# Kernel optimization log

Measured on AMD Instinct MI355X. Metric: run time of the kernel, lower is better.

Reference implementation:

```python
import jax, jax.numpy as jnp
import numpy as np

ROPE_BASE = 10000.0
ROPE_SCALE = 1.0
ATTN_SCALE = 0.08838834764831845  # query_pre_attn_scalar = 128**-0.5
WINDOW = 1024                     # sliding_window_size
EPS = 1e-6                        # flax RMSNorm default epsilon


def rms_norm(x, scale):
    var = jnp.mean(jnp.square(x), axis=-1, keepdims=True)
    return x * jax.lax.rsqrt(var + EPS) * scale


def apply_rope(x, positions):
    # x: [B, T, n, H]; positions: [B, T]
    H = x.shape[-1]
    frac = jnp.arange(0, H, 2, dtype=jnp.float32) / H        # [H/2]
    timescale = ROPE_BASE ** frac                             # [H/2]
    sinusoid = positions[..., None].astype(jnp.float32) / timescale  # [B,T,H/2]
    sinusoid = sinusoid / ROPE_SCALE
    sin = jnp.sin(sinusoid)[:, :, None, :]                    # [B,T,1,H/2]
    cos = jnp.cos(sinusoid)[:, :, None, :]
    x1, x2 = jnp.split(x, 2, axis=-1)
    return jnp.concatenate([x1 * cos - x2 * sin, x2 * cos + x1 * sin], axis=-1).astype(x.dtype)


def setup_inputs() -> dict:
    key = jax.random.key(0)
    ks = jax.random.split(key, 4)
    B, T, D, N, K, H = 1, 4096, 2048, 16, 8, 128
    return {
        "x": jax.random.normal(ks[0], (B, T, D), jnp.float32),
        "q_kernel": jax.random.normal(ks[1], (N, D, H), jnp.float32) * (D ** -0.5),
        "kv_kernel": jax.random.normal(ks[2], (2, K, D, H), jnp.float32) * (D ** -0.5),
        "out_kernel": jax.random.normal(ks[3], (N, H, D), jnp.float32) * ((N * H) ** -0.5),
        "q_norm_scale": jnp.ones((H,), jnp.float32),
        "k_norm_scale": jnp.ones((H,), jnp.float32),
    }


def reference(x, q_kernel, kv_kernel, out_kernel, q_norm_scale, k_norm_scale):
    B, T, D = x.shape
    N, _, H = q_kernel.shape
    K = kv_kernel.shape[1]
    G = N // K  # query heads per kv head (GQA group size)

    # projections
    q = jnp.einsum('btd,ndh->btnh', x, q_kernel)          # [B,T,N,H]
    kv = jnp.einsum('bsd,ckdh->cbskh', x, kv_kernel)      # [2,B,S,K,H]
    k, v = kv[0], kv[1]

    # QK-RMSNorm
    q = rms_norm(q, q_norm_scale)
    k = rms_norm(k, k_norm_scale)

    # RoPE (prefill: positions = arange(T) for every batch row)
    positions = jnp.broadcast_to(jnp.arange(T)[None, :], (B, T))
    q = apply_rope(q, positions)
    k = apply_rope(k, positions)

    # causal + sliding-window mask [T,S]
    i = jnp.arange(T)[:, None]
    j = jnp.arange(T)[None, :]
    mask = (j <= i) & (i - j < WINDOW)

    # grouped attention: [B,T,K,G,H] x [B,S,K,H]
    qg = q.reshape(B, T, K, G, H)
    logits = jnp.einsum('btkgh,bskh->bkgts', qg * ATTN_SCALE, k)
    logits = jnp.where(mask[None, None, None], logits, jnp.finfo(logits.dtype).min)
    probs = jax.nn.softmax(logits, axis=-1)
    enc = jnp.einsum('bkgts,bskh->btkgh', probs, v).reshape(B, T, N, H)

    return jnp.einsum('btnh,nhd->btd', enc, out_kernel)
```

## Files before the change

kernel.cpp:

```cpp
#include <hip/hip_runtime.h>
#include <hip/hip_bf16.h>


#define DEVINL __device__ __forceinline__

typedef __attribute__((ext_vector_type(4))) float f32x4;
typedef __attribute__((ext_vector_type(8))) short s16x8;
typedef __attribute__((ext_vector_type(4))) unsigned int u32x4;

constexpr int T = 4096, D = 2048, NQ = 16, KH = 8, H = 128;
constexpr int NCOLS = 4096;
constexpr float EPS = 1e-6f;
constexpr float ATTN_SCALE = 0.08838834764831845f;
constexpr int WINDOW = 1024;

DEVINL unsigned short f2bf(float f) {
    union { float f; unsigned int u; } v; v.f = f;
    unsigned int u = v.u;
    return (unsigned short)((u + 0x7fffu + ((u >> 16) & 1u)) >> 16);
}
DEVINL float bf2f(unsigned short h) {
    union { unsigned int u; float f; } v; v.u = ((unsigned int)h) << 16;
    return v.f;
}
DEVINL void gload_lds16(const unsigned short* g, unsigned short* l) {
    __builtin_amdgcn_global_load_lds(
        (const __attribute__((address_space(1))) unsigned int*)g,
        (__attribute__((address_space(3))) unsigned int*)l, 16, 0, 0);
}

__global__ __launch_bounds__(256) void k_cvt_x(const float* __restrict__ x,
                                               unsigned short* __restrict__ xb, int n8) {
    int i = blockIdx.x * 256 + threadIdx.x;
    if (i >= n8) return;
    const float4* src = (const float4*)x + (long)i * 2;
    float4 a = src[0], b = src[1];
    s16x8 o;
    o[0] = (short)f2bf(a.x); o[1] = (short)f2bf(a.y);
    o[2] = (short)f2bf(a.z); o[3] = (short)f2bf(a.w);
    o[4] = (short)f2bf(b.x); o[5] = (short)f2bf(b.y);
    o[6] = (short)f2bf(b.z); o[7] = (short)f2bf(b.w);
    ((s16x8*)xb)[i] = o;
}

__global__ __launch_bounds__(256) void k_tr_cvt_f32(const float* __restrict__ src,
                                                    unsigned short* __restrict__ dst,
                                                    int R, int C, long srcSlab, long dstSlab) {
    __shared__ float tile[32][33];
    int slab = blockIdx.z;
    src += (long)slab * srcSlab; dst += (long)slab * dstSlab;
    int c0 = blockIdx.x * 32, r0 = blockIdx.y * 32;
    int tx = threadIdx.x, ty = threadIdx.y;
    #pragma unroll
    for (int i = 0; i < 32; i += 8)
        tile[ty + i][tx] = src[(long)(r0 + ty + i) * C + c0 + tx];
    __syncthreads();
    #pragma unroll
    for (int i = 0; i < 32; i += 8)
        dst[(long)(c0 + ty + i) * R + r0 + tx] = f2bf(tile[tx][ty + i]);
}

__global__ __launch_bounds__(256) void k_rope_table(float2* __restrict__ rt) {
    int idx = blockIdx.x * 256 + threadIdx.x;
    int t = idx >> 6, j = idx & 63;
    float inv = expf(-(float)j * (logf(10000.0f) / 64.0f));
    float a = (float)t * inv;
    float s, c;
    sincosf(a, &s, &c);
    rt[idx] = make_float2(c, s);
}

template <bool BF16OUT>
__global__ __launch_bounds__(256) void k_gemm_bt(const unsigned short* __restrict__ A,
                                                 const unsigned short* __restrict__ Bt,
                                                 void* __restrict__ Cout,
                                                 int M, int N, int K) {
    constexpr int BK = 64;
    __shared__ __align__(16) unsigned short As[128 * BK];
    __shared__ __align__(16) unsigned short Bs[128 * BK];

    int nwg = gridDim.x, bid = blockIdx.x;
    int cpx = nwg >> 3;
    int wg = (bid & 7) * cpx + (bid >> 3);
    int nbn = N >> 7;
    int bm = wg / nbn, bn = wg % nbn;

    int tid = threadIdx.x;
    int w = tid >> 6, l = tid & 63;
    int g = l >> 4, lr = l & 15;
    int wrow = (w >> 1) * 64, wcol = (w & 1) * 64;

    const unsigned short* Abase = A + (long)(bm * 128) * K;
    const unsigned short* Bbase = Bt + (long)(bn * 128) * K;

    f32x4 acc[4][4] = {};

    for (int k0 = 0; k0 < K; k0 += BK) {
        #pragma unroll
        for (int j = 0; j < 4; ++j) {
            int chunk = j * 256 + tid;
            int row = chunk >> 3, slot = chunk & 7;
            int sl = slot ^ (row & 7);
            gload_lds16(Abase + (long)row * K + k0 + sl * 8,
                        As + (j * 256 + w * 64) * 8);
        }
        #pragma unroll
        for (int j = 0; j < 4; ++j) {
            int chunk = j * 256 + tid;
            int row = chunk >> 3, slot = chunk & 7;
            int sl = slot ^ (row & 7);
            gload_lds16(Bbase + (long)row * K + k0 + sl * 8,
                        Bs + (j * 256 + w * 64) * 8);
        }
        __syncthreads();
        #pragma unroll
        for (int kk = 0; kk < 2; ++kk) {
            s16x8 af[4], bf[4];
            #pragma unroll
            for (int mi = 0; mi < 4; ++mi) {
                int row = wrow + mi * 16 + lr;
                int slot = (kk * 4 + g) ^ (row & 7);
                af[mi] = *(const s16x8*)(As + row * BK + slot * 8);
            }
            #pragma unroll
            for (int ni = 0; ni < 4; ++ni) {
                int row = wcol + ni * 16 + lr;
                int slot = (kk * 4 + g) ^ (row & 7);
                bf[ni] = *(const s16x8*)(Bs + row * BK + slot * 8);
            }
            #pragma unroll
            for (int mi = 0; mi < 4; ++mi)
                #pragma unroll
                for (int ni = 0; ni < 4; ++ni)
                    acc[mi][ni] = __builtin_amdgcn_mfma_f32_16x16x32_bf16(
                        af[mi], bf[ni], acc[mi][ni], 0, 0, 0);
        }
        __syncthreads();
    }

    int crow0 = bm * 128 + wrow + g * 4;
    int ccol0 = bn * 128 + wcol + lr;
    #pragma unroll
    for (int mi = 0; mi < 4; ++mi)
        #pragma unroll
        for (int ni = 0; ni < 4; ++ni)
            #pragma unroll
            for (int j = 0; j < 4; ++j) {
                long r = crow0 + mi * 16 + j;
                long c = ccol0 + ni * 16;
                if (BF16OUT)
                    ((unsigned short*)Cout)[r * N + c] = f2bf(acc[mi][ni][j]);
                else
                    ((float*)Cout)[r * N + c] = acc[mi][ni][j];
            }
}

__global__ __launch_bounds__(256) void k_normrope(const unsigned short* __restrict__ Cqkv,
                                                  const float* __restrict__ qscale,
                                                  const float* __restrict__ kscale,
                                                  const float2* __restrict__ rt,
                                                  unsigned short* __restrict__ qro,
                                                  unsigned short* __restrict__ ksw) {
    int w = threadIdx.x >> 6, l = threadIdx.x & 63;
    int rid = blockIdx.x * 4 + w;
    int head = rid >> 12;
    int t = rid & 4095;
    int col0 = (head < NQ) ? head * H : D + (head - NQ) * H;
    const unsigned short* row = Cqkv + (long)t * NCOLS + col0;
    float x1 = bf2f(row[l]), x2 = bf2f(row[l + 64]);
    float ss = x1 * x1 + x2 * x2;
    #pragma unroll
    for (int off = 1; off < 64; off <<= 1) ss += __shfl_xor(ss, off);
    float r = rsqrtf(ss * (1.0f / 128.0f) + EPS);
    const float* scale = (head < NQ) ? qscale : kscale;
    float y1 = x1 * r * scale[l], y2 = x2 * r * scale[l + 64];
    float2 cs = rt[t * 64 + l];
    float o1 = y1 * cs.x - y2 * cs.y;
    float o2 = y2 * cs.x + y1 * cs.y;
    if (head < NQ) {
        o1 *= ATTN_SCALE; o2 *= ATTN_SCALE;
        unsigned short* dst = qro + ((long)head * T + t) * H;
        dst[l] = f2bf(o1); dst[l + 64] = f2bf(o2);
    } else {
        unsigned short* dst = ksw + ((long)(head - NQ) * T + t) * H;
        int sx = (t & 7) << 3;
        dst[l ^ sx] = f2bf(o1); dst[(l + 64) ^ sx] = f2bf(o2);
    }
}

__global__ __launch_bounds__(256) void k_tr_v(const unsigned short* __restrict__ Cqkv,
                                              unsigned short* __restrict__ vt) {
    __shared__ unsigned short tile[32][33];
    int kh = blockIdx.z;
    int h0 = blockIdx.y * 32;
    int s0 = blockIdx.x * 32;
    int tx = threadIdx.x, ty = threadIdx.y;
    #pragma unroll
    for (int i = 0; i < 32; i += 8)
        tile[ty + i][tx] = Cqkv[(long)(s0 + ty + i) * NCOLS + 3072 + kh * H + h0 + tx];
    __syncthreads();
    #pragma unroll
    for (int i = 0; i < 32; i += 8)
        vt[((long)kh * H + h0 + ty + i) * T + s0 + tx] = tile[tx][ty + i];
}

__global__ __launch_bounds__(512) void k_attn(const unsigned short* __restrict__ qro,
                                              const unsigned short* __restrict__ ksw,
                                              const unsigned short* __restrict__ vt,
                                              unsigned short* __restrict__ enc) {
    __shared__ __align__(16) unsigned short Ks[64 * 128];
    __shared__ __align__(16) unsigned short Vs[128 * 72];
    __shared__ __align__(16) unsigned short Ps[8][16 * 72];

    int nwg = gridDim.x, bid = blockIdx.x;
    int cpx = nwg >> 3;
    int wg = (bid & 7) * cpx + (bid >> 3);
    int n = wg >> 5;
    int qblk = wg & 31;
    int kvh = n >> 1;
    int q0 = qblk * 128;

    int tid = threadIdx.x, w = tid >> 6, l = tid & 63;
    int g = l >> 4, lr = l & 15;
    int qw0 = q0 + w * 16;

    const unsigned short* Kb = ksw + (long)kvh * T * H;
    const unsigned short* Vb = vt + (long)kvh * H * T;

    s16x8 qf[4];
    const unsigned short* qrow = qro + ((long)n * T + qw0 + lr) * H;
    #pragma unroll
    for (int c = 0; c < 4; ++c)
        qf[c] = *(const s16x8*)(qrow + c * 32 + g * 8);

    float psum[4] = {};
    f32x4 acc[8] = {};

    int ts_lo = q0 - (WINDOW - 1);
    ts_lo = ts_lo < 0 ? 0 : (ts_lo & ~63);
    int ts_hi = q0 + 64;

    for (int ts = ts_lo; ts <= ts_hi; ts += 64) {
        #pragma unroll
        for (int j = 0; j < 2; ++j)
            gload_lds16(Kb + (long)ts * H + (j * 512 + tid) * 8,
                        Ks + (j * 512 + w * 64) * 8);
        u32x4 vreg[2];
        #pragma unroll
        for (int j = 0; j < 2; ++j) {
            int chunk = j * 512 + tid;
            int h = chunk >> 3, slot = chunk & 7;
            vreg[j] = *(const u32x4*)(Vb + (long)h * T + ts + slot * 8);
        }
        #pragma unroll
        for (int j = 0; j < 2; ++j) {
            int chunk = j * 512 + tid;
            int h = chunk >> 3, slot = chunk & 7;
            *(u32x4*)(Vs + h * 72 + slot * 8) = vreg[j];
        }
        __syncthreads();

        if (ts <= qw0 + 15 && ts + 63 >= qw0 - (WINDOW - 1)) {
            f32x4 sf[4];
            #pragma unroll
            for (int sh = 0; sh < 4; ++sh) {
                f32x4 s4 = {};
                int srow = sh * 16 + lr;
                int sx = srow & 7;
                #pragma unroll
                for (int c = 0; c < 4; ++c) {
                    int slot = (c * 4 + g) ^ sx;
                    s16x8 kf = *(const s16x8*)(Ks + srow * 128 + slot * 8);
                    s4 = __builtin_amdgcn_mfma_f32_16x16x32_bf16(qf[c], kf, s4, 0, 0, 0);
                }
                sf[sh] = s4;
            }
            bool needmask = (ts + 63 > qw0) || (ts < qw0 - (WINDOW - 16));
            if (needmask) {
                #pragma unroll
                for (int j = 0; j < 4; ++j) {
                    int q = qw0 + g * 4 + j;
                    #pragma unroll
                    for (int sh = 0; sh < 4; ++sh) {
                        int s = ts + sh * 16 + lr;
                        bool valid = (s <= q) && (q - s < WINDOW);
                        sf[sh][j] = valid ? sf[sh][j] : -1e30f;
                    }
                }
            }
            unsigned short* P = &Ps[w][0];
            #pragma unroll
            for (int j = 0; j < 4; ++j) {
                int prow = g * 4 + j;
                #pragma unroll
                for (int sh = 0; sh < 4; ++sh) {
                    float p = __expf(sf[sh][j]);
                    psum[j] += p;
                    P[prow * 72 + sh * 16 + lr] = f2bf(p);
                }
            }
            #pragma unroll
            for (int kk = 0; kk < 2; ++kk) {
                s16x8 pf = *(const s16x8*)(P + lr * 72 + kk * 32 + g * 8);
                #pragma unroll
                for (int hc = 0; hc < 8; ++hc) {
                    int h = hc * 16 + lr;
                    s16x8 vf = *(const s16x8*)(Vs + h * 72 + kk * 32 + g * 8);
                    acc[hc] = __builtin_amdgcn_mfma_f32_16x16x32_bf16(pf, vf, acc[hc], 0, 0, 0);
                }
            }
        }
        __syncthreads();
    }

    #pragma unroll
    for (int j = 0; j < 4; ++j) {
        float ps = psum[j];
        ps += __shfl_xor(ps, 1);
        ps += __shfl_xor(ps, 2);
        ps += __shfl_xor(ps, 4);
        ps += __shfl_xor(ps, 8);
        float inv = 1.0f / ps;
        long r = qw0 + g * 4 + j;
        unsigned short* dst = enc + r * (long)D + n * H;
        #pragma unroll
        for (int hc = 0; hc < 8; ++hc)
            dst[hc * 16 + lr] = f2bf(acc[hc][j] * inv);
    }
}

extern "C" void kernel_launch(void* const* d_in, const int* in_sizes, int n_in,
                              void* d_out, int out_size, void* d_ws, size_t ws_size,
                              hipStream_t stream) {
    const float* x   = (const float*)d_in[0];
    const float* qk  = (const float*)d_in[1];
    const float* kvk = (const float*)d_in[2];
    const float* ok  = (const float*)d_in[3];
    const float* qs  = (const float*)d_in[4];
    const float* ks  = (const float*)d_in[5];

    char* ws = (char*)d_ws;
    unsigned short* xb    = (unsigned short*)(ws);
    unsigned short* WqkvT = (unsigned short*)(ws + 16777216);
    unsigned short* WoT   = (unsigned short*)(ws + 33554432);
    unsigned short* Cqkv  = (unsigned short*)(ws + 41943040);
    unsigned short* qro   = (unsigned short*)(ws + 75497472);
    unsigned short* kswp  = (unsigned short*)(ws + 92274688);
    unsigned short* vt    = (unsigned short*)(ws + 100663296);
    unsigned short* enc   = (unsigned short*)(ws + 109051904);
    float2*         rt    = (float2*)(ws + 125829120);

    dim3 tb(32, 8);
    k_cvt_x<<<4096, 256, 0, stream>>>(x, xb, T * D / 8);
    k_tr_cvt_f32<<<dim3(4, 64, 16), tb, 0, stream>>>(qk, WqkvT, 2048, 128,
                                                     (long)2048 * 128, (long)128 * 2048);
    k_tr_cvt_f32<<<dim3(4, 64, 16), tb, 0, stream>>>(kvk, WqkvT + (long)2048 * 2048, 2048, 128,
                                                     (long)2048 * 128, (long)128 * 2048);
    k_tr_cvt_f32<<<dim3(64, 64, 1), tb, 0, stream>>>(ok, WoT, 2048, 2048, 0, 0);
    k_rope_table<<<T * 64 / 256, 256, 0, stream>>>(rt);
    k_gemm_bt<true><<<32 * 32, 256, 0, stream>>>(xb, WqkvT, Cqkv, T, NCOLS, D);
    k_normrope<<<24 * T / 4, 256, 0, stream>>>(Cqkv, qs, ks, rt, qro, kswp);
    k_tr_v<<<dim3(128, 4, 8), tb, 0, stream>>>(Cqkv, vt);
    k_attn<<<NQ * (T / 128), 512, 0, stream>>>(qro, kswp, vt, enc);
    k_gemm_bt<false><<<32 * 16, 256, 0, stream>>>(enc, WoT, d_out, T, D, D);
}
```

Before: 341.0 us.

## Replace GEMM with 8-wave 256-row tiles and 4-stage pipelined LDS loads

Replaces the 128x128 single-buffered GEMM with an 8-wave, 512-thread kernel using 256xBN tiles. Half-K slices are staged through a 4-slot LDS ring with explicit vmcnt waits and barriers, so global loads overlap the MFMA work, and MFMA sections run at raised wave priority. The larger tile gives more reuse per block, but the QKV and output GEMMs now launch only 256 blocks each, and the hand-scheduled waitcnt sequence is fragile.

```diff
diff --git a/kernel.cpp b/kernel.cpp
--- a/kernel.cpp
+++ b/kernel.cpp
@@ -70,80 +70,119 @@
     rt[idx] = make_float2(c, s);
 }
 
-template <bool BF16OUT>
-__global__ __launch_bounds__(256) void k_gemm_bt(const unsigned short* __restrict__ A,
-                                                 const unsigned short* __restrict__ Bt,
-                                                 void* __restrict__ Cout,
-                                                 int M, int N, int K) {
-    constexpr int BK = 64;
-    __shared__ __align__(16) unsigned short As[128 * BK];
-    __shared__ __align__(16) unsigned short Bs[128 * BK];
+template <bool BF16OUT, int BN>
+__global__ __launch_bounds__(512, 2) void k_gemm8(const unsigned short* __restrict__ A,
+                                                  const unsigned short* __restrict__ Bt,
+                                                  void* __restrict__ Cout,
+                                                  int M, int N, int K) {
+    constexpr int WN  = BN / 4;
+    constexpr int NR  = WN / 16;
+    constexpr int NF  = NR / 2;
+    constexpr int CHB = (BN * 4) / 512;
+    constexpr int VMC = CHB + 2;
+    constexpr int ASL = 256 * 32;
+    constexpr int BSL = BN * 32;
+    __shared__ __align__(16) unsigned short As[4 * ASL];
+    __shared__ __align__(16) unsigned short Bs[4 * BSL];
 
     int nwg = gridDim.x, bid = blockIdx.x;
     int cpx = nwg >> 3;
     int wg = (bid & 7) * cpx + (bid >> 3);
-    int nbn = N >> 7;
+    int nbn = N / BN;
     int bm = wg / nbn, bn = wg % nbn;
 
     int tid = threadIdx.x;
     int w = tid >> 6, l = tid & 63;
     int g = l >> 4, lr = l & 15;
-    int wrow = (w >> 1) * 64, wcol = (w & 1) * 64;
-
-    const unsigned short* Abase = A + (long)(bm * 128) * K;
-    const unsigned short* Bbase = Bt + (long)(bn * 128) * K;
-
-    f32x4 acc[4][4] = {};
-
-    for (int k0 = 0; k0 < K; k0 += BK) {
-        #pragma unroll
-        for (int j = 0; j < 4; ++j) {
-            int chunk = j * 256 + tid;
-            int row = chunk >> 3, slot = chunk & 7;
-            int sl = slot ^ (row & 7);
-            gload_lds16(Abase + (long)row * K + k0 + sl * 8,
-                        As + (j * 256 + w * 64) * 8);
-        }
-        #pragma unroll
-        for (int j = 0; j < 4; ++j) {
-            int chunk = j * 256 + tid;
-            int row = chunk >> 3, slot = chunk & 7;
-            int sl = slot ^ (row & 7);
-            gload_lds16(Bbase + (long)row * K + k0 + sl * 8,
-                        Bs + (j * 256 + w * 64) * 8);
-        }
-        __syncthreads();
-        #pragma unroll
-        for (int kk = 0; kk < 2; ++kk) {
-            s16x8 af[4], bf[4];
+    int wm = w >> 2, wn = w & 3;
+
+    const unsigned short* Ab = A + (long)(bm * 256) * K;
+    const unsigned short* Bb = Bt + (long)(bn * BN) * K;
+
+    f32x4 acc[8][NR] = {};
+    s16x8 a[8], b[NF];
+
+    auto stA = [&](int slot, int tt, int h) {
+        #pragma unroll
+        for (int j = 0; j < 2; ++j) {
+            int c = j * 512 + tid;
+            int row = c >> 2, sp = c & 3;
+            int s = sp ^ ((row >> 1) & 3);
+            gload_lds16(Ab + (long)row * K + tt * 64 + h * 32 + s * 8,
+                        As + slot * ASL + (j * 512 + w * 64) * 8);
+        }
+    };
+    auto stB = [&](int slot, int tt, int h) {
+        #pragma unroll
+        for (int j = 0; j < CHB; ++j) {
+            int c = j * 512 + tid;
+            int row = c >> 2, sp = c & 3;
+            int s = sp ^ ((row >> 1) & 3);
+            gload_lds16(Bb + (long)row * K + tt * 64 + h * 32 + s * 8,
+                        Bs + slot * BSL + (j * 512 + w * 64) * 8);
+        }
+    };
+    auto rdA = [&](int slot) {
+        #pragma unroll
+        for (int mi = 0; mi < 8; ++mi) {
+            int row = wm * 128 + mi * 16 + lr;
+            int sp = g ^ ((row >> 1) & 3);
+            a[mi] = *(const s16x8*)(As + slot * ASL + row * 32 + sp * 8);
+        }
+    };
+    auto rdB = [&](int slot, int nh) {
+        #pragma unroll
+        for (int f = 0; f < NF; ++f) {
+            int row = wn * WN + (nh * NF + f) * 16 + lr;
+            int sp = g ^ ((row >> 1) & 3);
+            b[f] = *(const s16x8*)(Bs + slot * BSL + row * 32 + sp * 8);
+        }
+    };
+    auto mm = [&](int nh) {
+        __builtin_amdgcn_s_setprio(1);
+        #pragma unroll
+        for (int mi = 0; mi < 8; ++mi)
             #pragma unroll
-            for (int mi = 0; mi < 4; ++mi) {
-                int row = wrow + mi * 16 + lr;
-                int slot = (kk * 4 + g) ^ (row & 7);
-                af[mi] = *(const s16x8*)(As + row * BK + slot * 8);
-            }
-            #pragma unroll
-            for (int ni = 0; ni < 4; ++ni) {
-                int row = wcol + ni * 16 + lr;
-                int slot = (kk * 4 + g) ^ (row & 7);
-                bf[ni] = *(const s16x8*)(Bs + row * BK + slot * 8);
-            }
-            #pragma unroll
-            for (int mi = 0; mi < 4; ++mi)
-                #pragma unroll
-                for (int ni = 0; ni < 4; ++ni)
-                    acc[mi][ni] = __builtin_amdgcn_mfma_f32_16x16x32_bf16(
-                        af[mi], bf[ni], acc[mi][ni], 0, 0, 0);
-        }
-        __syncthreads();
+            for (int f = 0; f < NF; ++f)
+                acc[mi][nh * NF + f] = __builtin_amdgcn_mfma_f32_16x16x32_bf16(
+                    a[mi], b[f], acc[mi][nh * NF + f], 0, 0, 0);
+        __builtin_amdgcn_s_setprio(0);
+    };
+#define GVM()  asm volatile("s_waitcnt vmcnt(%0)" :: "i"(VMC) : "memory")
+#define GBAR() { __builtin_amdgcn_s_barrier(); asm volatile("" ::: "memory"); }
+
+    stA(0, 0, 0); stB(0, 0, 0); stA(1, 0, 1); stB(1, 0, 1);
+    stA(2, 1, 0); stB(2, 1, 0); stA(3, 1, 1);
+
+    int KT = K >> 6;
+    for (int u = 0; u < (KT >> 1); ++u) {
+        int te = 2 * u, to = te + 1;
+        GVM(); GBAR();
+        rdA(0); rdB(0, 0); stB(3, to, 1);      mm(0);
+        GBAR();
+        rdB(0, 1);         stA(0, te + 2, 0);  mm(1);
+        GVM(); GBAR();
+        rdA(1); rdB(1, 0); stB(0, te + 2, 0);  mm(0);
+        GBAR();
+        rdB(1, 1);         stA(1, te + 2, 1);  mm(1);
+        GVM(); GBAR();
+        rdA(2); rdB(2, 0); stB(1, te + 2, 1);  mm(0);
+        GBAR();
+        rdB(2, 1);         stA(2, to + 2, 0);  mm(1);
+        GVM(); GBAR();
+        rdA(3); rdB(3, 0); stB(2, to + 2, 0);  mm(0);
+        GBAR();
+        rdB(3, 1);         stA(3, to + 2, 1);  mm(1);
     }
-
-    int crow0 = bm * 128 + wrow + g * 4;
-    int ccol0 = bn * 128 + wcol + lr;
-    #pragma unroll
-    for (int mi = 0; mi < 4; ++mi)
-        #pragma unroll
-        for (int ni = 0; ni < 4; ++ni)
+#undef GVM
+#undef GBAR
+
+    int crow0 = bm * 256 + wm * 128 + g * 4;
+    int ccol0 = bn * BN + wn * WN + lr;
+    #pragma unroll
+    for (int mi = 0; mi < 8; ++mi)
+        #pragma unroll
+        for (int ni = 0; ni < NR; ++ni)
             #pragma unroll
             for (int j = 0; j < 4; ++j) {
                 long r = crow0 + mi * 16 + j;
@@ -358,9 +397,9 @@
                                                      (long)2048 * 128, (long)128 * 2048);
     k_tr_cvt_f32<<<dim3(64, 64, 1), tb, 0, stream>>>(ok, WoT, 2048, 2048, 0, 0);
     k_rope_table<<<T * 64 / 256, 256, 0, stream>>>(rt);
-    k_gemm_bt<true><<<32 * 32, 256, 0, stream>>>(xb, WqkvT, Cqkv, T, NCOLS, D);
+    k_gemm8<true, 256><<<256, 512, 0, stream>>>(xb, WqkvT, Cqkv, T, NCOLS, D);
     k_normrope<<<24 * T / 4, 256, 0, stream>>>(Cqkv, qs, ks, rt, qro, kswp);
     k_tr_v<<<dim3(128, 4, 8), tb, 0, stream>>>(Cqkv, vt);
     k_attn<<<NQ * (T / 128), 512, 0, stream>>>(qro, kswp, vt, enc);
-    k_gemm_bt<false><<<32 * 16, 256, 0, stream>>>(enc, WoT, d_out, T, D, D);
-}
+    k_gemm8<false, 128><<<256, 512, 0, stream>>>(enc, WoT, d_out, T, D, D);
+}
```

Result: faster. 328.4 us (-3.7%).
